# Performance work log

Hardware: AMD Instinct MI355X
Metric: run time of the kernel (lower is better)

The kernel has to match this reference:

```python
import jax, jax.numpy as jnp
import numpy as np

N = 3072
E = 32 * N
H = 8
IN_F = 64
OUT_F = 16
ALPHA = 0.2  # LeakyReLU slope
NEG_INF = -9e15


def setup_inputs() -> dict:
    key = jax.random.key(0)
    k1, k2, k3, k4, k5 = jax.random.split(key, 5)
    h = jax.random.normal(k1, (N, IN_F), dtype=jnp.float32)
    edge_index = jax.random.randint(k2, (2, E), 0, N, dtype=jnp.int64)
    S = jax.random.uniform(k3, (N, N), dtype=jnp.float32)
    W = jax.random.normal(k4, (H, IN_F, OUT_F), dtype=jnp.float32) * 0.2
    a = jax.random.normal(k5, (H, 2 * OUT_F, 1), dtype=jnp.float32) * 0.3
    raw_gamma = jnp.ones((H,), dtype=jnp.float32)
    return {"h": h, "edge_index": edge_index, "S": S, "W": W, "a": a, "raw_gamma": raw_gamma}


def reference(h, edge_index, S, W, a, raw_gamma):
    n = h.shape[0]
    # dense adjacency from edge list (to_dense_adj semantics: adj[src, dst] += 1)
    adj = jnp.zeros((n, n), dtype=h.dtype).at[edge_index[0], edge_index[1]].add(1.0)
    # per-head projection: Wh [H, N, O]
    Wh = jnp.einsum('nf,hfo->hno', h, W)
    o = W.shape[2]
    a1 = a[:, :o, 0]  # [H, O]
    a2 = a[:, o:, 0]  # [H, O]
    e1 = jnp.einsum('hno,ho->hn', Wh, a1)  # Wh @ a[:O]
    e2 = jnp.einsum('hno,ho->hn', Wh, a2)  # Wh @ a[O:]
    e = jax.nn.leaky_relu(e1[:, :, None] + e2[:, None, :], ALPHA)  # [H, N, N]
    att = jnp.where(adj[None] > 0, e, jnp.asarray(NEG_INF, e.dtype))
    gamma = jax.nn.softplus(raw_gamma)  # [H], non-negative gate
    att = att * (1.0 + gamma[:, None, None] * S[None])
    att = jax.nn.softmax(att, axis=-1)  # row softmax (dim=1 of [N, N])
    # dropout is identity in eval mode
    h_prime = jnp.einsum('hnm,hmo->hno', att, Wh)  # [H, N, O]
    h_prime = jax.nn.elu(h_prime)  # concat=True per head
    # concat heads along feature dim -> [N, H*O]
    return jnp.transpose(h_prime, (1, 0, 2)).reshape(n, -1)
```

## Files before the change

### kernel.cpp

```cpp
#include <hip/hip_runtime.h>
#include <math.h>

#define N_NODES 3072
#define H_HEADS 8
#define IN_FEAT 64
#define OUT_FEAT 16
#define WORDS_PER_ROW 96
#define MAXD 96
#define SCATTER_BLOCKS 384
#define WH_NPB 16
#define WH_BLOCKS (N_NODES / WH_NPB)

__launch_bounds__(256)
__global__ void scatter_and_wh_kernel(const int* __restrict__ ei, int E,
                                      int* __restrict__ cnt,
                                      unsigned int* __restrict__ bits,
                                      int* __restrict__ adj,
                                      const float* __restrict__ hfeat,
                                      const float* __restrict__ W,
                                      const float* __restrict__ a,
                                      float* __restrict__ Wh,
                                      float* __restrict__ e1t,
                                      float* __restrict__ e2t) {
    __shared__ __align__(16) float Wt[H_HEADS][OUT_FEAT][68];
    __shared__ __align__(16) float hs[WH_NPB][IN_FEAT];

    int tid = threadIdx.x;
    if (blockIdx.x < SCATTER_BLOCKS) {
        int e = blockIdx.x * 256 + tid;
        if (e < E) {
            int r = ei[e];
            int c = ei[E + e];
            unsigned int bit = 1u << (c & 31);
            unsigned int old = atomicOr(&bits[r * WORDS_PER_ROW + (c >> 5)], bit);
            if (!(old & bit)) {
                int pos = atomicAdd(&cnt[r], 1);
                if (pos < MAXD) adj[r * MAXD + pos] = c;
            }
        }
        return;
    }

    int node_base = (blockIdx.x - SCATTER_BLOCKS) * WH_NPB;
    for (int idx = tid; idx < H_HEADS * IN_FEAT * OUT_FEAT; idx += 256) {
        int hh = idx >> 10, f = (idx >> 4) & 63, o = idx & 15;
        Wt[hh][o][f] = W[idx];
    }
    for (int idx = tid; idx < WH_NPB * IN_FEAT; idx += 256)
        hs[idx >> 6][idx & 63] = hfeat[node_base * IN_FEAT + idx];
    __syncthreads();

    int ng = tid >> 7;
    int hh = (tid >> 4) & 7;
    int o  = tid & 15;
    float a1v = a[hh * 2 * OUT_FEAT + o];
    float a2v = a[hh * 2 * OUT_FEAT + OUT_FEAT + o];

    float4 w[16];
#pragma unroll
    for (int q = 0; q < 16; ++q)
        w[q] = *(const float4*)&Wt[hh][o][4 * q];

    for (int n = ng; n < WH_NPB; n += 2) {
        float acc = 0.f;
#pragma unroll
        for (int q = 0; q < 16; ++q) {
            float4 hv = *(const float4*)&hs[n][4 * q];
            acc = fmaf(hv.x, w[q].x, acc);
            acc = fmaf(hv.y, w[q].y, acc);
            acc = fmaf(hv.z, w[q].z, acc);
            acc = fmaf(hv.w, w[q].w, acc);
        }
        int node = node_base + n;
        Wh[(hh * N_NODES + node) * OUT_FEAT + o] = acc;
        float p1 = acc * a1v, p2 = acc * a2v;
#pragma unroll
        for (int m = 1; m < 16; m <<= 1) {
            p1 += __shfl_xor(p1, m, 64);
            p2 += __shfl_xor(p2, m, 64);
        }
        if (o == 0) {
            e1t[node * H_HEADS + hh] = p1;
            e2t[node * H_HEADS + hh] = p2;
        }
    }
}

__launch_bounds__(256)
__global__ void gat_main_kernel(const int* __restrict__ cnts,
                                const int* __restrict__ adj,
                                const float* __restrict__ S,
                                const float* __restrict__ Wh,
                                const float* __restrict__ e1t,
                                const float* __restrict__ e2t,
                                const float* __restrict__ raw_gamma,
                                float* __restrict__ out) {
    __shared__ int lds_j[MAXD];
    __shared__ float lds_s[MAXD];
    __shared__ float lds_e2h[H_HEADS][MAXD];
    __shared__ float lds_p[H_HEADS][MAXD];
    __shared__ int fb_j;
    int i = blockIdx.x;
    int tid = threadIdx.x;
    int wave = tid >> 6, lane = tid & 63;

    int cnt = cnts[i];
    if (cnt > MAXD) cnt = MAXD;

    if (tid < cnt) {
        int j = adj[i * MAXD + tid];
        lds_j[tid] = j;
        lds_s[tid] = S[i * N_NODES + j];
        const float4* ep = (const float4*)&e2t[j * H_HEADS];
        float4 ea = ep[0], eb = ep[1];
        lds_e2h[0][tid] = ea.x; lds_e2h[1][tid] = ea.y;
        lds_e2h[2][tid] = ea.z; lds_e2h[3][tid] = ea.w;
        lds_e2h[4][tid] = eb.x; lds_e2h[5][tid] = eb.y;
        lds_e2h[6][tid] = eb.z; lds_e2h[7][tid] = eb.w;
    }
    __syncthreads();

    if (cnt == 0) {
        if (wave == 0) {
            float bm = 3.4e38f; int bj = 0;
            for (int j = lane; j < N_NODES; j += 64) {
                float sv = S[i * N_NODES + j];
                if (sv < bm) { bm = sv; bj = j; }
            }
            for (int m = 1; m < 64; m <<= 1) {
                float bm2 = __shfl_xor(bm, m, 64);
                int bj2 = __shfl_xor(bj, m, 64);
                if (bm2 < bm || (bm2 == bm && bj2 < bj)) { bm = bm2; bj = bj2; }
            }
            if (lane == 0) fb_j = bj;
        }
        __syncthreads();
        int jj = fb_j;
        if (tid < H_HEADS * OUT_FEAT) {
            int h2 = tid >> 4, o2 = tid & 15;
            float x = Wh[(h2 * N_NODES + jj) * OUT_FEAT + o2];
            out[i * (H_HEADS * OUT_FEAT) + h2 * OUT_FEAT + o2] =
                x > 0.f ? x : __expf(x) - 1.f;
        }
        return;
    }

    int half = lane >> 5;
    int hl = lane & 31;
    int hh = wave * 2 + half;
    float g = log1pf(__expf(raw_gamma[hh]));
    float e1v = e1t[i * H_HEADS + hh];
    float l = 0.f;
    for (int k = hl; k < cnt; k += 32) {
        float x = e1v + lds_e2h[hh][k];
        x = x > 0.f ? x : 0.2f * x;
        float p = __expf(x * (1.f + g * lds_s[k]));
        lds_p[hh][k] = p;
        l += p;
    }
#pragma unroll
    for (int m = 1; m < 32; m <<= 1)
        l += __shfl_xor(l, m, 64);

    int kgrp = hl >> 4, o = hl & 15;
    float acc = 0.f;
    for (int kk = kgrp; kk < cnt; kk += 2)
        acc = fmaf(lds_p[hh][kk], Wh[(hh * N_NODES + lds_j[kk]) * OUT_FEAT + o], acc);
    acc += __shfl_xor(acc, 16, 64);
    if (kgrp == 0) {
        float x = acc / l;
        out[i * (H_HEADS * OUT_FEAT) + hh * OUT_FEAT + o] =
            x > 0.f ? x : __expf(x) - 1.f;
    }
}

extern "C" void kernel_launch(void* const* d_in, const int* in_sizes, int n_in,
                              void* d_out, int out_size, void* d_ws, size_t ws_size,
                              hipStream_t stream) {
    const float* hfeat = (const float*)d_in[0];
    const int* ei      = (const int*)d_in[1];
    const float* S     = (const float*)d_in[2];
    const float* W     = (const float*)d_in[3];
    const float* a     = (const float*)d_in[4];
    const float* rg    = (const float*)d_in[5];
    float* out = (float*)d_out;

    char* ws = (char*)d_ws;
    int* cnt = (int*)ws;
    unsigned int* bits = (unsigned int*)(ws + 12288);
    int* adj = (int*)(ws + 12288 + 1179648);
    float* Wh = (float*)(ws + 12288 + 2 * 1179648);
    float* e1t = (float*)(ws + 12288 + 2 * 1179648 + 1572864);
    float* e2t = e1t + N_NODES * H_HEADS;

    hipMemsetAsync(ws, 0, 12288 + 1179648, stream);

    int E = in_sizes[1] / 2;
    scatter_and_wh_kernel<<<SCATTER_BLOCKS + WH_BLOCKS, 256, 0, stream>>>(
        ei, E, cnt, bits, adj, hfeat, W, a, Wh, e1t, e2t);

    gat_main_kernel<<<N_NODES, 256, 0, stream>>>(cnt, adj, S, Wh, e1t, e2t, rg, out);
}
```

Before: 120.4 us.

## Build per-row neighbor lists from bitmask via wave prefix-scan instead of atomic counters

The scatter phase now only sets adjacency bits with atomicOr, dropping the dependent atomicAdd on a per-row counter and the scattered adjacency-list write. The main kernel instead reads each row's 96-word bitmask, runs a wave-level popcount prefix scan, and expands set bits into a sorted neighbor list in LDS. This removes contended atomics and a workspace array, at the cost of extra serial bit-extraction work per block before the softmax stage. Neighbor order becomes sorted by column, which changes the floating-point summation order.

```diff
diff --git a/kernel.cpp b/kernel.cpp
--- a/kernel.cpp
+++ b/kernel.cpp
@@ -13,9 +13,7 @@
 
 __launch_bounds__(256)
 __global__ void scatter_and_wh_kernel(const int* __restrict__ ei, int E,
-                                      int* __restrict__ cnt,
                                       unsigned int* __restrict__ bits,
-                                      int* __restrict__ adj,
                                       const float* __restrict__ hfeat,
                                       const float* __restrict__ W,
                                       const float* __restrict__ a,
@@ -31,12 +29,7 @@
         if (e < E) {
             int r = ei[e];
             int c = ei[E + e];
-            unsigned int bit = 1u << (c & 31);
-            unsigned int old = atomicOr(&bits[r * WORDS_PER_ROW + (c >> 5)], bit);
-            if (!(old & bit)) {
-                int pos = atomicAdd(&cnt[r], 1);
-                if (pos < MAXD) adj[r * MAXD + pos] = c;
-            }
+            atomicOr(&bits[r * WORDS_PER_ROW + (c >> 5)], 1u << (c & 31));
         }
         return;
     }
@@ -87,8 +80,7 @@
 }
 
 __launch_bounds__(256)
-__global__ void gat_main_kernel(const int* __restrict__ cnts,
-                                const int* __restrict__ adj,
+__global__ void gat_main_kernel(const unsigned int* __restrict__ bits,
                                 const float* __restrict__ S,
                                 const float* __restrict__ Wh,
                                 const float* __restrict__ e1t,
@@ -99,17 +91,45 @@
     __shared__ float lds_s[MAXD];
     __shared__ float lds_e2h[H_HEADS][MAXD];
     __shared__ float lds_p[H_HEADS][MAXD];
+    __shared__ int lds_cnt;
     __shared__ int fb_j;
     int i = blockIdx.x;
     int tid = threadIdx.x;
     int wave = tid >> 6, lane = tid & 63;
 
-    int cnt = cnts[i];
+    if (wave == 0) {
+        unsigned int w0 = bits[i * WORDS_PER_ROW + lane];
+        unsigned int w1 = (lane < WORDS_PER_ROW - 64)
+                              ? bits[i * WORDS_PER_ROW + 64 + lane] : 0u;
+        int c = __popc(w0) + __popc(w1);
+        int s = c;
+#pragma unroll
+        for (int d = 1; d < 64; d <<= 1) {
+            int v = __shfl_up(s, d, 64);
+            if (lane >= d) s += v;
+        }
+        int off = s - c;
+        if (lane == 63) lds_cnt = s;
+        unsigned int b = w0;
+        int base = lane << 5;
+        while (b) {
+            int bit = __ffs(b) - 1; b &= b - 1;
+            if (off < MAXD) lds_j[off] = base + bit;
+            ++off;
+        }
+        b = w1; base = (64 + lane) << 5;
+        while (b) {
+            int bit = __ffs(b) - 1; b &= b - 1;
+            if (off < MAXD) lds_j[off] = base + bit;
+            ++off;
+        }
+    }
+    __syncthreads();
+    int cnt = lds_cnt;
     if (cnt > MAXD) cnt = MAXD;
 
     if (tid < cnt) {
-        int j = adj[i * MAXD + tid];
-        lds_j[tid] = j;
+        int j = lds_j[tid];
         lds_s[tid] = S[i * N_NODES + j];
         const float4* ep = (const float4*)&e2t[j * H_HEADS];
         float4 ea = ep[0], eb = ep[1];
@@ -186,18 +206,16 @@
     float* out = (float*)d_out;
 
     char* ws = (char*)d_ws;
-    int* cnt = (int*)ws;
-    unsigned int* bits = (unsigned int*)(ws + 12288);
-    int* adj = (int*)(ws + 12288 + 1179648);
-    float* Wh = (float*)(ws + 12288 + 2 * 1179648);
-    float* e1t = (float*)(ws + 12288 + 2 * 1179648 + 1572864);
+    unsigned int* bits = (unsigned int*)ws;
+    float* Wh = (float*)(ws + 1179648);
+    float* e1t = (float*)(ws + 1179648 + 1572864);
     float* e2t = e1t + N_NODES * H_HEADS;
 
-    hipMemsetAsync(ws, 0, 12288 + 1179648, stream);
+    hipMemsetAsync(bits, 0, (size_t)N_NODES * WORDS_PER_ROW * 4, stream);
 
     int E = in_sizes[1] / 2;
     scatter_and_wh_kernel<<<SCATTER_BLOCKS + WH_BLOCKS, 256, 0, stream>>>(
-        ei, E, cnt, bits, adj, hfeat, W, a, Wh, e1t, e2t);
-
-    gat_main_kernel<<<N_NODES, 256, 0, stream>>>(cnt, adj, S, Wh, e1t, e2t, rg, out);
+        ei, E, bits, hfeat, W, a, Wh, e1t, e2t);
+
+    gat_main_kernel<<<N_NODES, 256, 0, stream>>>(bits, S, Wh, e1t, e2t, rg, out);
 }
```

Result: faster. 112.3 us (-6.8%).
